# Optimization experiments

Measured on AMD Instinct MI355X. Metric: run time of the kernel, lower is better.

Reference implementation:

```python
import jax, jax.numpy as jnp
import numpy as np

NUM_CLASSES = 80
SCORE_THRESH = 0.5
NMS_THRESH = 0.5
TOP_K = 200  # max candidates kept per (image, class) before greedy NMS


def setup_inputs() -> dict:
    key = jax.random.key(0)
    k1, k2, k3 = jax.random.split(key, 3)
    B, A, HW, C = 8, 3, 5776, NUM_CLASSES  # 608-input YOLOv4 P3 level: 76*76
    # well-formed boxes in [0,1]: x1y1 + positive wh
    xy = jax.random.uniform(k1, (B, A, HW, 2)) * 0.8
    wh = jax.random.uniform(k2, (B, A, HW, 2)) * 0.2 + 0.01
    boxes = jnp.concatenate([xy, xy + wh], axis=-1)
    scores = jax.random.uniform(k3, (B, A, HW, C))
    return {"boxes": boxes, "scores": scores}


def _pairwise_iou(b):
    # b: [K, 4] (x1, y1, x2, y2) -> IoU matrix [K, K] (union mode)
    x1, y1, x2, y2 = b[:, 0], b[:, 1], b[:, 2], b[:, 3]
    area = (x2 - x1) * (y2 - y1)
    xx1 = jnp.maximum(x1[:, None], x1[None, :])
    yy1 = jnp.maximum(y1[:, None], y1[None, :])
    xx2 = jnp.minimum(x2[:, None], x2[None, :])
    yy2 = jnp.minimum(y2[:, None], y2[None, :])
    inter = jnp.maximum(0.0, xx2 - xx1) * jnp.maximum(0.0, yy2 - yy1)
    return inter / (area[:, None] + area[None, :] - inter)


def _nms_one(boxes, scores):
    # boxes: [N, 4], scores: [N] -> top-K candidates with greedy-NMS keep mask
    s = jnp.where(scores > SCORE_THRESH, scores, -jnp.inf)  # score threshold filter
    top_s, idx = jax.lax.top_k(s, TOP_K)                    # descending, like argsort()[::-1]
    b = boxes[idx]                                          # [K, 4]
    valid = jnp.isfinite(top_s)
    iou = _pairwise_iou(b)                                  # [K, K]

    def body(keep, i):
        # if box i survives, suppress all lower-scored boxes with IoU > thresh
        sup = keep[i] & (iou[i] > NMS_THRESH) & (jnp.arange(TOP_K) > i)
        return keep & ~sup, None

    keep, _ = jax.lax.scan(body, valid, jnp.arange(TOP_K))
    return b, top_s, keep


def reference(boxes, scores):
    B, A, HW, _ = boxes.shape
    C = scores.shape[-1]
    b = boxes.reshape(B, A * HW, 4)
    s = scores.reshape(B, A * HW, C)
    per_img = jax.vmap(lambda bb, ss: jax.vmap(_nms_one, in_axes=(None, 1))(bb, ss))
    boxes_k, scores_k, keep = per_img(b, s)  # [B,C,K,4], [B,C,K], [B,C,K]
    cls = jnp.broadcast_to(jnp.arange(C, dtype=boxes.dtype)[None, :, None], keep.shape)
    out_box = jnp.where(keep[..., None], boxes_k, 0.0)
    out_score = jnp.where(keep, scores_k, 0.0)
    out_cls = jnp.where(keep, cls, 0.0)
    # padded detections [B, C, K, 6] = (x1, y1, x2, y2, score, class_id)
    return jnp.concatenate([out_box, out_score[..., None], out_cls[..., None]], axis=-1)
```

## Files before the change

### kernel.cpp

```cpp
#include <hip/hip_runtime.h>
#include <stdint.h>

#define B_IMG  8
#define NANCH  17328
#define NCLS   80
#define TOPK   200
#define NTHR   256
#define CHUNK  64
#define NCHK   ((NANCH + CHUNK - 1) / CHUNK)
#define NCHKP  272
#define SLOT   24
#define ALLK_CAP 2608
#define THRESH_HI 0.9f

__device__ __forceinline__ void hist_add(float s, unsigned int* hist) {
  if (s > 0.5f) {
    unsigned int bin = (__float_as_uint(s) - 0x3F000000u) >> 15;
    if (bin > 255u) bin = 255u;
    atomicAdd(&hist[bin], 1u);
  }
}

__global__ __launch_bounds__(NTHR) void scatter_k(
    const float* __restrict__ scores,
    unsigned char* __restrict__ cnt2,
    unsigned long long* __restrict__ cand) {
  const int nb = blockIdx.x;
  const int b  = blockIdx.y;
  const int tid = threadIdx.x;
  const int wv = tid >> 6, lane = tid & 63;
  const int n0 = nb * CHUNK;

  __shared__ float tile[CHUNK][81];

  const int nrow = (NANCH - n0 < CHUNK) ? (NANCH - n0) : CHUNK;
  const int nf4 = nrow * (NCLS / 4);
  const float4* src4 = (const float4*)(scores + (size_t)(b * NANCH + n0) * NCLS);
  for (int f = tid; f < nf4; f += NTHR) {
    float4 v = src4[f];
    int n = f / 20, c4 = (f - n * 20) * 4;
    tile[n][c4] = v.x; tile[n][c4 + 1] = v.y;
    tile[n][c4 + 2] = v.z; tile[n][c4 + 3] = v.w;
  }
  __syncthreads();

  const bool rv = (lane < nrow);
  const unsigned long long lt = (1ull << lane) - 1ull;
  const int cbase = wv * 20;
#pragma unroll 4
  for (int cc = 0; cc < 20; ++cc) {
    const int c = cbase + cc;
    const int bc = b * NCLS + c;
    float s = rv ? tile[lane][c] : 0.f;
    const bool cd = (s > THRESH_HI);
    unsigned long long bal = __ballot(cd);
    if (cd) {
      unsigned int r = (unsigned int)__popcll(bal & lt);
      if (r < SLOT)
        cand[((size_t)bc * NCHK + nb) * SLOT + r] =
            ((unsigned long long)__float_as_uint(s) << 32) |
            (unsigned long long)(0xFFFFFFFFu - (unsigned int)(n0 + lane));
    }
    if (lane == 0)
      cnt2[(size_t)bc * NCHKP + nb] = (unsigned char)__popcll(bal);
  }
}

__global__ __launch_bounds__(NTHR) void stage1_k(
    const float* __restrict__ scores, const float* __restrict__ boxes,
    const unsigned char* __restrict__ cnt2, const unsigned long long* __restrict__ cand,
    float4* __restrict__ stagedBox, unsigned long long* __restrict__ stagedKey) {
  const int bc = blockIdx.x;
  const int b = bc / NCLS;
  const int c = bc - b * NCLS;
  const int tid = threadIdx.x;

  __shared__ unsigned long long allk[ALLK_CAP];
  __shared__ unsigned long long selk[512];
  __shared__ unsigned int hist[256];
  __shared__ unsigned int sh_cutbits;
  __shared__ int sh_m, sh_sel, sh_bad;

  for (int j = tid; j < 256; j += NTHR) hist[j] = 0u;
  if (tid == 0) { sh_m = 0; sh_sel = 0; sh_bad = 0; }
  __syncthreads();

  for (int ch = tid; ch < NCHK; ch += NTHR) {
    unsigned int ci = (unsigned int)cnt2[(size_t)bc * NCHKP + ch];
    if (ci > SLOT) { sh_bad = 1; continue; }
    if (ci == 0u) continue;
    int base = atomicAdd(&sh_m, (int)ci);
    if (base + (int)ci > ALLK_CAP) { sh_bad = 1; continue; }
    const unsigned long long* cb = cand + ((size_t)bc * NCHK + ch) * SLOT;
    for (unsigned int j = 0; j < ci; ++j) {
      unsigned long long k = cb[j];
      allk[base + j] = k;
      unsigned int bin = ((unsigned int)(k >> 32) - 0x3F000000u) >> 15;
      if (bin > 255u) bin = 255u;
      atomicAdd(&hist[bin], 1u);
    }
  }
  __syncthreads();

  const int Mall = sh_m;
  const bool fast = (!sh_bad) && (Mall >= TOPK);

  if (fast) {
    if (tid < 64) {
      int base = 255 - 4 * tid;
      int s4 = (int)(hist[base] + hist[base - 1] + hist[base - 2] + hist[base - 3]);
      int cum = s4;
      for (int d = 1; d < 64; d <<= 1) {
        int o = __shfl_up(cum, d, 64);
        if (tid >= d) cum += o;
      }
      unsigned long long bal = __ballot(cum >= TOPK);
      if (bal == 0ull) {
        if (tid == 0) sh_cutbits = 0x3F000000u;
      } else {
        int l0 = __builtin_ctzll(bal);
        if (tid == l0) {
          unsigned int acc = (unsigned int)(cum - s4);
          int cutbin = base - 3;
          for (int k = 0; k < 4; ++k) {
            acc += hist[base - k];
            if (acc >= TOPK) { cutbin = base - k; break; }
          }
          sh_cutbits = 0x3F000000u + ((unsigned int)cutbin << 15);
        }
      }
    }
    __syncthreads();
    const unsigned int cutbits = sh_cutbits;

    for (int j = tid; j < Mall; j += NTHR) {
      unsigned long long k = allk[j];
      if ((unsigned int)(k >> 32) >= cutbits) {
        int slot = atomicAdd(&sh_sel, 1);
        if (slot < 512) selk[slot] = k;
      }
    }
    __syncthreads();
  } else {
    for (int j = tid; j < 256; j += NTHR) hist[j] = 0u;
    __syncthreads();
    const float* src = scores + (size_t)b * NANCH * NCLS + c;
    for (int i = tid; i < NANCH; i += NTHR) hist_add(src[(size_t)i * NCLS], hist);
    __syncthreads();

    if (tid == 0) {
      unsigned int acc = 0;
      int cut = 0;
      for (int bin = 255; bin >= 0; --bin) {
        acc += hist[bin];
        if (acc >= TOPK) { cut = bin; break; }
      }
      sh_cutbits = 0x3F000000u + ((unsigned int)cut << 15);
    }
    __syncthreads();
    const unsigned int cutbits = sh_cutbits;

    for (int i = tid; i < NANCH; i += NTHR) {
      float s = src[(size_t)i * NCLS];
      if (s > 0.5f && __float_as_uint(s) >= cutbits) {
        int slot = atomicAdd(&sh_sel, 1);
        if (slot < 512)
          selk[slot] = ((unsigned long long)__float_as_uint(s) << 32) |
                       (unsigned long long)(0xFFFFFFFFu - (unsigned int)i);
      }
    }
    __syncthreads();
  }

  int M = sh_sel; if (M > 512) M = 512;
  const int S = (M <= 256) ? 256 : 512;
  for (int j = M + tid; j < S; j += NTHR) selk[j] = 0ull;

  for (int size = 2; size <= S; size <<= 1) {
    for (int st = size >> 1; st > 0; st >>= 1) {
      __syncthreads();
      for (int t = tid; t < (S >> 1); t += NTHR) {
        int lo = 2 * t - (t & (st - 1));
        int hi = lo + st;
        bool desc = ((lo & size) == 0);
        unsigned long long a = selk[lo], bb = selk[hi];
        if ((a < bb) == desc) { selk[lo] = bb; selk[hi] = a; }
      }
    }
  }
  __syncthreads();

  {
    unsigned long long key = selk[tid];
    int valid = (tid < TOPK) && (key != 0ull);
    unsigned int idx = 0xFFFFFFFFu - (unsigned int)(key & 0xFFFFFFFFull);
    float4 bx = make_float4(0.f, 0.f, 0.f, 0.f);
    if (valid) bx = ((const float4*)boxes)[(size_t)b * NANCH + idx];
    stagedBox[(size_t)bc * 256 + tid] = bx;
    stagedKey[(size_t)bc * 256 + tid] = key;
  }
}

__global__ __launch_bounds__(NTHR) void supbuild_k(
    const float4* __restrict__ stagedBox,
    unsigned long long* __restrict__ supg) {
  const int blk = blockIdx.x;
  const int h = blk & 3;
  const int bc = blk >> 2;
  const int tid = threadIdx.x;
  const int wv = tid >> 6, lane = tid & 63;

  __shared__ float sx1[256], sy1[256], sx2[256], sy2[256], sar[256];

  if (tid < 256) {
    float4 bx = stagedBox[(size_t)bc * 256 + tid];
    sx1[tid] = bx.x; sy1[tid] = bx.y; sx2[tid] = bx.z; sy2[tid] = bx.w;
    sar[tid] = __fmul_rn(bx.z - bx.x, bx.w - bx.y);
  }
  __syncthreads();

  float jx1[4], jy1[4], jx2[4], jy2[4], ja[4];
#pragma unroll
  for (int r = 0; r < 4; ++r) {
    int j = (r << 6) | lane;
    jx1[r] = sx1[j]; jy1[r] = sy1[j]; jx2[r] = sx2[j]; jy2[r] = sy2[j];
    ja[r] = sar[j];
  }

  for (int k = 0; k < 13; ++k) {
    const int i = 16 * k + 4 * wv + h;
    if (i >= TOPK) break;
    const float xi1 = sx1[i], yi1 = sy1[i], xi2 = sx2[i], yi2 = sy2[i];
    const float ai = sar[i];
    unsigned long long w[4];
#pragma unroll
    for (int r = 0; r < 4; ++r) {
      unsigned long long word = 0ull;
      if ((r << 6) + 63 > i) {
        const int j = (r << 6) | lane;
        const bool vp = (j > i) && (j < TOPK);
        float xx1 = fmaxf(xi1, jx1[r]);
        float yy1 = fmaxf(yi1, jy1[r]);
        float xx2 = fminf(xi2, jx2[r]);
        float yy2 = fminf(yi2, jy2[r]);
        float iw = fmaxf(0.f, __fsub_rn(xx2, xx1));
        float ih = fmaxf(0.f, __fsub_rn(yy2, yy1));
        float inter = __fmul_rn(iw, ih);
        float denom = __fsub_rn(__fadd_rn(ai, ja[r]), inter);
        float q = __fmul_rn(inter, __builtin_amdgcn_rcpf(denom));
        bool s = vp && (q > 0.5f);
        bool gbad = vp && (fabsf(q - 0.5f) < 1e-5f);
        if (__ballot(gbad)) {
          if (gbad) s = __fdiv_rn(inter, denom) > 0.5f;
        }
        word = __ballot(s);
      }
      w[r] = word;
    }
    if (lane == 0) {
      ulonglong2* dst = (ulonglong2*)(supg + ((size_t)bc * TOPK + i) * 4);
      ulonglong2 t0; t0.x = w[0]; t0.y = w[1];
      ulonglong2 t1; t1.x = w[2]; t1.y = w[3];
      dst[0] = t0; dst[1] = t1;
    }
  }
}

__global__ __launch_bounds__(NTHR) void scanemit_k(
    const float4* __restrict__ stagedBox, const unsigned long long* __restrict__ stagedKey,
    const unsigned long long* __restrict__ supg, float* __restrict__ out) {
  const int bc = blockIdx.x;
  const int c = bc - (bc / NCLS) * NCLS;
  const int tid = threadIdx.x;

  __shared__ float sx1[256], sy1[256], sx2[256], sy2[256], ssc[256];
  __shared__ int skeep[256];
  __shared__ __align__(16) unsigned long long sup[TOPK][4];
  __shared__ __align__(16) float eout[TOPK * 6];

  {
    unsigned long long key = stagedKey[(size_t)bc * 256 + tid];
    float4 bx = stagedBox[(size_t)bc * 256 + tid];
    int valid = (tid < TOPK) && (key != 0ull);
    sx1[tid] = bx.x; sy1[tid] = bx.y; sx2[tid] = bx.z; sy2[tid] = bx.w;
    ssc[tid] = valid ? __uint_as_float((unsigned int)(key >> 32)) : 0.f;
    skeep[tid] = valid;
  }
  {
    const ulonglong2* src = (const ulonglong2*)(supg + (size_t)bc * TOPK * 4);
    ulonglong2* dst = (ulonglong2*)&sup[0][0];
    for (int f = tid; f < TOPK * 2; f += NTHR) dst[f] = src[f];
  }
  __syncthreads();

  if (tid < 64) {
    unsigned long long k0 = __ballot(skeep[tid] != 0);
    unsigned long long k1 = __ballot(skeep[64 + tid] != 0);
    unsigned long long k2 = __ballot(skeep[128 + tid] != 0);
    unsigned long long k3 = __ballot(skeep[192 + tid] != 0);
#define NMS_SCAN_WORD(KW, BASE, CNT)                                     \
    _Pragma("unroll 8")                                                  \
    for (int li = 0; li < (CNT); ++li) {                                 \
      const ulonglong2* s2p =                                            \
          reinterpret_cast<const ulonglong2*>(&sup[(BASE) + li][0]);     \
      ulonglong2 sa = s2p[0];                                            \
      ulonglong2 sb = s2p[1];                                            \
      unsigned long long m = 0ull - ((KW >> li) & 1ull);                 \
      k0 &= ~(sa.x & m); k1 &= ~(sa.y & m);                              \
      k2 &= ~(sb.x & m); k3 &= ~(sb.y & m);                              \
    }
    NMS_SCAN_WORD(k0, 0, 64)
    NMS_SCAN_WORD(k1, 64, 64)
    NMS_SCAN_WORD(k2, 128, 64)
    NMS_SCAN_WORD(k3, 192, 8)
#undef NMS_SCAN_WORD
    skeep[tid]        = (int)((k0 >> tid) & 1ull);
    skeep[64 + tid]   = (int)((k1 >> tid) & 1ull);
    skeep[128 + tid]  = (int)((k2 >> tid) & 1ull);
    skeep[192 + tid]  = (int)((k3 >> tid) & 1ull);
  }
  __syncthreads();

  if (tid < TOPK) {
    int kp = skeep[tid];
    eout[tid * 6 + 0] = kp ? sx1[tid] : 0.f;
    eout[tid * 6 + 1] = kp ? sy1[tid] : 0.f;
    eout[tid * 6 + 2] = kp ? sx2[tid] : 0.f;
    eout[tid * 6 + 3] = kp ? sy2[tid] : 0.f;
    eout[tid * 6 + 4] = kp ? ssc[tid] : 0.f;
    eout[tid * 6 + 5] = kp ? (float)c : 0.f;
  }
  __syncthreads();

  float4* out4 = (float4*)(out + (size_t)bc * (TOPK * 6));
  const float4* e4 = (const float4*)eout;
  for (int f = tid; f < (TOPK * 6) / 4; f += NTHR) out4[f] = e4[f];
}

__global__ __launch_bounds__(NTHR) void select_nms_k(
    const float* __restrict__ boxes, const float* __restrict__ scores,
    float* __restrict__ out) {
  const int blk = blockIdx.x;
  const int b = blk / NCLS;
  const int c = blk - b * NCLS;
  const int tid = threadIdx.x;

  __shared__ unsigned int hist[256];
  __shared__ unsigned long long keys[1024];
  __shared__ float sx1[TOPK], sy1[TOPK], sx2[TOPK], sy2[TOPK], sar[TOPK], ssc[TOPK];
  __shared__ int skeep[TOPK];
  __shared__ unsigned int sh_cutbits;
  __shared__ int sh_m;

  const float* src = scores + (size_t)b * NANCH * NCLS + c;

  for (int j = tid; j < 256; j += NTHR) hist[j] = 0;
  if (tid == 0) sh_m = 0;
  __syncthreads();

  for (int i = tid; i < NANCH; i += NTHR) hist_add(src[(size_t)i * NCLS], hist);
  __syncthreads();

  if (tid == 0) {
    unsigned int acc = 0;
    int cut = 0;
    for (int bin = 255; bin >= 0; --bin) {
      acc += hist[bin];
      if (acc >= TOPK) { cut = bin; break; }
    }
    sh_cutbits = 0x3F000000u + ((unsigned int)cut << 15);
  }
  __syncthreads();
  const unsigned int cutbits = sh_cutbits;

  for (int i = tid; i < NANCH; i += NTHR) {
    float s = src[(size_t)i * NCLS];
    if (s > 0.5f && __float_as_uint(s) >= cutbits) {
      int slot = atomicAdd(&sh_m, 1);
      if (slot < 1024)
        keys[slot] = ((unsigned long long)__float_as_uint(s) << 32) |
                     (unsigned long long)(0xFFFFFFFFu - (unsigned int)i);
    }
  }
  __syncthreads();
  int M = sh_m; if (M > 1024) M = 1024;
  for (int j = M + tid; j < 1024; j += NTHR) keys[j] = 0ull;

  for (int size = 2; size <= 1024; size <<= 1) {
    for (int st = size >> 1; st > 0; st >>= 1) {
      __syncthreads();
      for (int t = tid; t < 512; t += NTHR) {
        int lo = 2 * t - (t & (st - 1));
        int hi = lo + st;
        bool desc = ((lo & size) == 0);
        unsigned long long a = keys[lo], bb = keys[hi];
        if ((a < bb) == desc) { keys[lo] = bb; keys[hi] = a; }
      }
    }
  }
  __syncthreads();

  if (tid < TOPK) {
    unsigned long long key = keys[tid];
    int valid = (key != 0ull);
    float sc = __uint_as_float((unsigned int)(key >> 32));
    unsigned int idx = 0xFFFFFFFFu - (unsigned int)(key & 0xFFFFFFFFull);
    float4 bx = make_float4(0.f, 0.f, 0.f, 0.f);
    if (valid) bx = ((const float4*)boxes)[(size_t)b * NANCH + idx];
    sx1[tid] = bx.x; sy1[tid] = bx.y; sx2[tid] = bx.z; sy2[tid] = bx.w;
    sar[tid] = __fmul_rn(bx.z - bx.x, bx.w - bx.y);
    ssc[tid] = valid ? sc : 0.f;
    skeep[tid] = valid;
  }
  __syncthreads();

  if (tid < 64) {
    const int lane = tid;
    float x1v[4], y1v[4], x2v[4], y2v[4], av[4];
    int km = 0;
#pragma unroll
    for (int r = 0; r < 4; ++r) {
      int j = lane + (r << 6);
      if (j < TOPK) {
        x1v[r] = sx1[j]; y1v[r] = sy1[j]; x2v[r] = sx2[j]; y2v[r] = sy2[j];
        av[r] = sar[j];
        if (skeep[j]) km |= (1 << r);
      } else {
        x1v[r] = 0.f; y1v[r] = 0.f; x2v[r] = 0.f; y2v[r] = 0.f; av[r] = 0.f;
      }
    }
#pragma unroll
    for (int ri = 0; ri < 4; ++ri) {
      const int imax = (ri == 3) ? (TOPK - 192) : 64;
      for (int li = 0; li < imax; ++li) {
        const int i = (ri << 6) + li;
        int kmi = __shfl(km, li, 64);
        if (!((kmi >> ri) & 1)) continue;
        float xi1 = __shfl(x1v[ri], li, 64);
        float yi1 = __shfl(y1v[ri], li, 64);
        float xi2 = __shfl(x2v[ri], li, 64);
        float yi2 = __shfl(y2v[ri], li, 64);
        float ai  = __shfl(av[ri],  li, 64);
#pragma unroll
        for (int r = 0; r < 4; ++r) {
          int j = lane + (r << 6);
          if (j > i && j < TOPK && ((km >> r) & 1)) {
            float xx1 = fmaxf(xi1, x1v[r]);
            float yy1 = fmaxf(yi1, y1v[r]);
            float xx2 = fminf(xi2, x2v[r]);
            float yy2 = fminf(yi2, y2v[r]);
            float iw = fmaxf(0.f, __fsub_rn(xx2, xx1));
            float ih = fmaxf(0.f, __fsub_rn(yy2, yy1));
            float inter = __fmul_rn(iw, ih);
            float denom = __fsub_rn(__fadd_rn(ai, av[r]), inter);
            float iou = __fdiv_rn(inter, denom);
            if (iou > 0.5f) km &= ~(1 << r);
          }
        }
      }
    }
#pragma unroll
    for (int r = 0; r < 4; ++r) {
      int j = lane + (r << 6);
      if (j < TOPK) skeep[j] = (km >> r) & 1;
    }
  }
  __syncthreads();

  const size_t base = ((size_t)b * NCLS + c) * (TOPK * 6);
  for (int f = tid; f < TOPK * 6; f += NTHR) {
    int k = f / 6, comp = f - k * 6;
    float v = 0.f;
    if (skeep[k]) {
      switch (comp) {
        case 0: v = sx1[k]; break;
        case 1: v = sy1[k]; break;
        case 2: v = sx2[k]; break;
        case 3: v = sy2[k]; break;
        case 4: v = ssc[k]; break;
        default: v = (float)c; break;
      }
    }
    out[base + f] = v;
  }
}

extern "C" void kernel_launch(void* const* d_in, const int* in_sizes, int n_in,
                              void* d_out, int out_size, void* d_ws, size_t ws_size,
                              hipStream_t stream) {
  (void)in_sizes; (void)n_in; (void)out_size;
  const float* boxes  = (const float*)d_in[0];
  const float* scores = (const float*)d_in[1];
  float* out = (float*)d_out;

  const int NBC = B_IMG * NCLS;
  const size_t need_c2  = (size_t)NBC * NCHKP;
  const size_t need_cd  = (size_t)NBC * NCHK * SLOT * sizeof(uint64_t);
  const size_t need_sb  = (size_t)NBC * 256 * sizeof(float4);
  const size_t need_sk  = (size_t)NBC * 256 * sizeof(uint64_t);
  const size_t need_sp  = (size_t)NBC * TOPK * 4 * sizeof(uint64_t);
  const size_t need = need_c2 + need_cd + need_sb + need_sk + need_sp;

  if (ws_size >= need) {
    char* w = (char*)d_ws;
    unsigned char* cnt2           = (unsigned char*)w;         w += need_c2;
    unsigned long long* cand      = (unsigned long long*)w;    w += need_cd;
    float4* stagedBox             = (float4*)w;                w += need_sb;
    unsigned long long* stagedKey = (unsigned long long*)w;    w += need_sk;
    unsigned long long* supg      = (unsigned long long*)w;

    scatter_k<<<dim3(NCHK, B_IMG), NTHR, 0, stream>>>(scores, cnt2, cand);
    stage1_k<<<NBC, NTHR, 0, stream>>>(scores, boxes, cnt2, cand, stagedBox, stagedKey);
    supbuild_k<<<NBC * 4, NTHR, 0, stream>>>(stagedBox, supg);
    scanemit_k<<<NBC, NTHR, 0, stream>>>(stagedBox, stagedKey, supg, out);
  } else {
    select_nms_k<<<NBC, NTHR, 0, stream>>>(boxes, scores, out);
  }
}
```

Measured before the change: 77.75 us.

## Fuse selection, suppression-matrix build and scan into one 1024-thread kernel

Merges stage1_k, supbuild_k and scanemit_k into a single mega_k kernel with 1024 threads per (image, class) block. Staged boxes, keys and the suppression bitmask now stay in shared memory instead of round-tripping through global workspace. This removes two kernel launches and the global traffic between them. In exchange, each block uses much more shared memory and is larger, which lowers occupancy. The IoU matrix for one class is now built by 16 waves in one block rather than spread across four blocks.

```diff
diff --git a/kernel.cpp b/kernel.cpp
--- a/kernel.cpp
+++ b/kernel.cpp
@@ -6,6 +6,7 @@
 #define NCLS   80
 #define TOPK   200
 #define NTHR   256
+#define NTHRM  1024
 #define CHUNK  64
 #define NCHK   ((NANCH + CHUNK - 1) / CHUNK)
 #define NCHKP  272
@@ -66,26 +67,31 @@
   }
 }
 
-__global__ __launch_bounds__(NTHR) void stage1_k(
+__global__ __launch_bounds__(NTHRM) void mega_k(
     const float* __restrict__ scores, const float* __restrict__ boxes,
     const unsigned char* __restrict__ cnt2, const unsigned long long* __restrict__ cand,
-    float4* __restrict__ stagedBox, unsigned long long* __restrict__ stagedKey) {
+    float* __restrict__ out) {
   const int bc = blockIdx.x;
   const int b = bc / NCLS;
   const int c = bc - b * NCLS;
   const int tid = threadIdx.x;
+  const int wv = tid >> 6, lane = tid & 63;
 
   __shared__ unsigned long long allk[ALLK_CAP];
   __shared__ unsigned long long selk[512];
   __shared__ unsigned int hist[256];
+  __shared__ float sx1[256], sy1[256], sx2[256], sy2[256], sar[256], ssc[256];
+  __shared__ int skeep[256];
+  __shared__ __align__(16) unsigned long long sup[TOPK][4];
+  __shared__ __align__(16) float eout[TOPK * 6];
   __shared__ unsigned int sh_cutbits;
   __shared__ int sh_m, sh_sel, sh_bad;
 
-  for (int j = tid; j < 256; j += NTHR) hist[j] = 0u;
+  if (tid < 256) hist[tid] = 0u;
   if (tid == 0) { sh_m = 0; sh_sel = 0; sh_bad = 0; }
   __syncthreads();
 
-  for (int ch = tid; ch < NCHK; ch += NTHR) {
+  for (int ch = tid; ch < NCHK; ch += NTHRM) {
     unsigned int ci = (unsigned int)cnt2[(size_t)bc * NCHKP + ch];
     if (ci > SLOT) { sh_bad = 1; continue; }
     if (ci == 0u) continue;
@@ -133,7 +139,7 @@
     __syncthreads();
     const unsigned int cutbits = sh_cutbits;
 
-    for (int j = tid; j < Mall; j += NTHR) {
+    for (int j = tid; j < Mall; j += NTHRM) {
       unsigned long long k = allk[j];
       if ((unsigned int)(k >> 32) >= cutbits) {
         int slot = atomicAdd(&sh_sel, 1);
@@ -142,10 +148,10 @@
     }
     __syncthreads();
   } else {
-    for (int j = tid; j < 256; j += NTHR) hist[j] = 0u;
+    if (tid < 256) hist[tid] = 0u;
     __syncthreads();
     const float* src = scores + (size_t)b * NANCH * NCLS + c;
-    for (int i = tid; i < NANCH; i += NTHR) hist_add(src[(size_t)i * NCLS], hist);
+    for (int i = tid; i < NANCH; i += NTHRM) hist_add(src[(size_t)i * NCLS], hist);
     __syncthreads();
 
     if (tid == 0) {
@@ -160,7 +166,7 @@
     __syncthreads();
     const unsigned int cutbits = sh_cutbits;
 
-    for (int i = tid; i < NANCH; i += NTHR) {
+    for (int i = tid; i < NANCH; i += NTHRM) {
       float s = src[(size_t)i * NCLS];
       if (s > 0.5f && __float_as_uint(s) >= cutbits) {
         int slot = atomicAdd(&sh_sel, 1);
@@ -174,12 +180,12 @@
 
   int M = sh_sel; if (M > 512) M = 512;
   const int S = (M <= 256) ? 256 : 512;
-  for (int j = M + tid; j < S; j += NTHR) selk[j] = 0ull;
+  for (int j = M + tid; j < S; j += NTHRM) selk[j] = 0ull;
 
   for (int size = 2; size <= S; size <<= 1) {
     for (int st = size >> 1; st > 0; st >>= 1) {
       __syncthreads();
-      for (int t = tid; t < (S >> 1); t += NTHR) {
+      for (int t = tid; t < (S >> 1); t += NTHRM) {
         int lo = 2 * t - (t & (st - 1));
         int hi = lo + st;
         bool desc = ((lo & size) == 0);
@@ -190,106 +196,64 @@
   }
   __syncthreads();
 
-  {
+  if (tid < 256) {
     unsigned long long key = selk[tid];
     int valid = (tid < TOPK) && (key != 0ull);
     unsigned int idx = 0xFFFFFFFFu - (unsigned int)(key & 0xFFFFFFFFull);
     float4 bx = make_float4(0.f, 0.f, 0.f, 0.f);
     if (valid) bx = ((const float4*)boxes)[(size_t)b * NANCH + idx];
-    stagedBox[(size_t)bc * 256 + tid] = bx;
-    stagedKey[(size_t)bc * 256 + tid] = key;
-  }
-}
-
-__global__ __launch_bounds__(NTHR) void supbuild_k(
-    const float4* __restrict__ stagedBox,
-    unsigned long long* __restrict__ supg) {
-  const int blk = blockIdx.x;
-  const int h = blk & 3;
-  const int bc = blk >> 2;
-  const int tid = threadIdx.x;
-  const int wv = tid >> 6, lane = tid & 63;
-
-  __shared__ float sx1[256], sy1[256], sx2[256], sy2[256], sar[256];
-
-  if (tid < 256) {
-    float4 bx = stagedBox[(size_t)bc * 256 + tid];
     sx1[tid] = bx.x; sy1[tid] = bx.y; sx2[tid] = bx.z; sy2[tid] = bx.w;
     sar[tid] = __fmul_rn(bx.z - bx.x, bx.w - bx.y);
-  }
-  __syncthreads();
-
-  float jx1[4], jy1[4], jx2[4], jy2[4], ja[4];
-#pragma unroll
-  for (int r = 0; r < 4; ++r) {
-    int j = (r << 6) | lane;
-    jx1[r] = sx1[j]; jy1[r] = sy1[j]; jx2[r] = sx2[j]; jy2[r] = sy2[j];
-    ja[r] = sar[j];
-  }
-
-  for (int k = 0; k < 13; ++k) {
-    const int i = 16 * k + 4 * wv + h;
-    if (i >= TOPK) break;
-    const float xi1 = sx1[i], yi1 = sy1[i], xi2 = sx2[i], yi2 = sy2[i];
-    const float ai = sar[i];
-    unsigned long long w[4];
-#pragma unroll
-    for (int r = 0; r < 4; ++r) {
-      unsigned long long word = 0ull;
-      if ((r << 6) + 63 > i) {
-        const int j = (r << 6) | lane;
-        const bool vp = (j > i) && (j < TOPK);
-        float xx1 = fmaxf(xi1, jx1[r]);
-        float yy1 = fmaxf(yi1, jy1[r]);
-        float xx2 = fminf(xi2, jx2[r]);
-        float yy2 = fminf(yi2, jy2[r]);
-        float iw = fmaxf(0.f, __fsub_rn(xx2, xx1));
-        float ih = fmaxf(0.f, __fsub_rn(yy2, yy1));
-        float inter = __fmul_rn(iw, ih);
-        float denom = __fsub_rn(__fadd_rn(ai, ja[r]), inter);
-        float q = __fmul_rn(inter, __builtin_amdgcn_rcpf(denom));
-        bool s = vp && (q > 0.5f);
-        bool gbad = vp && (fabsf(q - 0.5f) < 1e-5f);
-        if (__ballot(gbad)) {
-          if (gbad) s = __fdiv_rn(inter, denom) > 0.5f;
-        }
-        word = __ballot(s);
-      }
-      w[r] = word;
-    }
-    if (lane == 0) {
-      ulonglong2* dst = (ulonglong2*)(supg + ((size_t)bc * TOPK + i) * 4);
-      ulonglong2 t0; t0.x = w[0]; t0.y = w[1];
-      ulonglong2 t1; t1.x = w[2]; t1.y = w[3];
-      dst[0] = t0; dst[1] = t1;
-    }
-  }
-}
-
-__global__ __launch_bounds__(NTHR) void scanemit_k(
-    const float4* __restrict__ stagedBox, const unsigned long long* __restrict__ stagedKey,
-    const unsigned long long* __restrict__ supg, float* __restrict__ out) {
-  const int bc = blockIdx.x;
-  const int c = bc - (bc / NCLS) * NCLS;
-  const int tid = threadIdx.x;
-
-  __shared__ float sx1[256], sy1[256], sx2[256], sy2[256], ssc[256];
-  __shared__ int skeep[256];
-  __shared__ __align__(16) unsigned long long sup[TOPK][4];
-  __shared__ __align__(16) float eout[TOPK * 6];
-
-  {
-    unsigned long long key = stagedKey[(size_t)bc * 256 + tid];
-    float4 bx = stagedBox[(size_t)bc * 256 + tid];
-    int valid = (tid < TOPK) && (key != 0ull);
-    sx1[tid] = bx.x; sy1[tid] = bx.y; sx2[tid] = bx.z; sy2[tid] = bx.w;
     ssc[tid] = valid ? __uint_as_float((unsigned int)(key >> 32)) : 0.f;
     skeep[tid] = valid;
   }
+  __syncthreads();
+
   {
-    const ulonglong2* src = (const ulonglong2*)(supg + (size_t)bc * TOPK * 4);
-    ulonglong2* dst = (ulonglong2*)&sup[0][0];
-    for (int f = tid; f < TOPK * 2; f += NTHR) dst[f] = src[f];
+    float jx1[4], jy1[4], jx2[4], jy2[4], ja[4];
+#pragma unroll
+    for (int r = 0; r < 4; ++r) {
+      int j = (r << 6) | lane;
+      jx1[r] = sx1[j]; jy1[r] = sy1[j]; jx2[r] = sx2[j]; jy2[r] = sy2[j];
+      ja[r] = sar[j];
+    }
+    for (int k = 0; k < 13; ++k) {
+      const int i = (k << 4) + wv;
+      if (i >= TOPK) break;
+      const float xi1 = sx1[i], yi1 = sy1[i], xi2 = sx2[i], yi2 = sy2[i];
+      const float ai = sar[i];
+      unsigned long long w[4];
+#pragma unroll
+      for (int r = 0; r < 4; ++r) {
+        unsigned long long word = 0ull;
+        if ((r << 6) + 63 > i) {
+          const int j = (r << 6) | lane;
+          const bool vp = (j > i) && (j < TOPK);
+          float xx1 = fmaxf(xi1, jx1[r]);
+          float yy1 = fmaxf(yi1, jy1[r]);
+          float xx2 = fminf(xi2, jx2[r]);
+          float yy2 = fminf(yi2, jy2[r]);
+          float iw = fmaxf(0.f, __fsub_rn(xx2, xx1));
+          float ih = fmaxf(0.f, __fsub_rn(yy2, yy1));
+          float inter = __fmul_rn(iw, ih);
+          float denom = __fsub_rn(__fadd_rn(ai, ja[r]), inter);
+          float q = __fmul_rn(inter, __builtin_amdgcn_rcpf(denom));
+          bool s = vp && (q > 0.5f);
+          bool gbad = vp && (fabsf(q - 0.5f) < 1e-5f);
+          if (__ballot(gbad)) {
+            if (gbad) s = __fdiv_rn(inter, denom) > 0.5f;
+          }
+          word = __ballot(s);
+        }
+        w[r] = word;
+      }
+      if (lane == 0) {
+        ulonglong2* dst = (ulonglong2*)&sup[i][0];
+        ulonglong2 t0; t0.x = w[0]; t0.y = w[1];
+        ulonglong2 t1; t1.x = w[2]; t1.y = w[3];
+        dst[0] = t0; dst[1] = t1;
+      }
+    }
   }
   __syncthreads();
 
@@ -334,7 +298,7 @@
 
   float4* out4 = (float4*)(out + (size_t)bc * (TOPK * 6));
   const float4* e4 = (const float4*)eout;
-  for (int f = tid; f < (TOPK * 6) / 4; f += NTHR) out4[f] = e4[f];
+  for (int f = tid; f < (TOPK * 6) / 4; f += NTHRM) out4[f] = e4[f];
 }
 
 __global__ __launch_bounds__(NTHR) void select_nms_k(
@@ -496,23 +460,15 @@
   const int NBC = B_IMG * NCLS;
   const size_t need_c2  = (size_t)NBC * NCHKP;
   const size_t need_cd  = (size_t)NBC * NCHK * SLOT * sizeof(uint64_t);
-  const size_t need_sb  = (size_t)NBC * 256 * sizeof(float4);
-  const size_t need_sk  = (size_t)NBC * 256 * sizeof(uint64_t);
-  const size_t need_sp  = (size_t)NBC * TOPK * 4 * sizeof(uint64_t);
-  const size_t need = need_c2 + need_cd + need_sb + need_sk + need_sp;
+  const size_t need = need_c2 + need_cd;
 
   if (ws_size >= need) {
     char* w = (char*)d_ws;
-    unsigned char* cnt2           = (unsigned char*)w;         w += need_c2;
-    unsigned long long* cand      = (unsigned long long*)w;    w += need_cd;
-    float4* stagedBox             = (float4*)w;                w += need_sb;
-    unsigned long long* stagedKey = (unsigned long long*)w;    w += need_sk;
-    unsigned long long* supg      = (unsigned long long*)w;
+    unsigned char* cnt2      = (unsigned char*)w;       w += need_c2;
+    unsigned long long* cand = (unsigned long long*)w;
 
     scatter_k<<<dim3(NCHK, B_IMG), NTHR, 0, stream>>>(scores, cnt2, cand);
-    stage1_k<<<NBC, NTHR, 0, stream>>>(scores, boxes, cnt2, cand, stagedBox, stagedKey);
-    supbuild_k<<<NBC * 4, NTHR, 0, stream>>>(stagedBox, supg);
-    scanemit_k<<<NBC, NTHR, 0, stream>>>(stagedBox, stagedKey, supg, out);
+    mega_k<<<NBC, NTHRM, 0, stream>>>(scores, boxes, cnt2, cand, out);
   } else {
     select_nms_k<<<NBC, NTHR, 0, stream>>>(boxes, scores, out);
   }
```

Result: slower. 107.1 us (+37.7%).
